# Optimization experiments

Hardware: AMD Instinct MI355X
Metric: run time of the kernel (lower is better)

Reference implementation:

```python
import jax, jax.numpy as jnp
import numpy as np

B, S, IN, H, OUT = 64, 512, 1024, 512, 512
EPS = 1e-5
ADAPTIVE_RATE = 0.01


def setup_inputs() -> dict:
    key = jax.random.key(0)
    ks = iter(jax.random.split(key, 64))

    def rn(shape, scale):
        return (jax.random.normal(next(ks), shape, jnp.float32) * scale)

    d = {}
    d["x"] = jax.random.normal(next(ks), (B, S, IN), jnp.float32)
    d["context"] = jax.random.normal(next(ks), (B, H), jnp.float32)
    d["state_importance"] = jnp.ones((1, H), jnp.float32)
    # embedding
    d["W_emb"], d["b_emb"] = rn((H, IN), 0.02), rn((H,), 0.01)
    # core layers: Linear + BatchNorm1d (gamma=1, beta=0 torch init)
    d["W0"], d["b0"] = rn((H, H), 0.03), rn((H,), 0.01)
    d["g0"], d["bt0"] = jnp.ones((H,), jnp.float32), jnp.zeros((H,), jnp.float32)
    d["W1"], d["b1"] = rn((H, H), 0.03), rn((H,), 0.01)
    d["g1"], d["bt1"] = jnp.ones((H,), jnp.float32), jnp.zeros((H,), jnp.float32)
    # two LSTMCells (hidden -> hidden), torch gate order i,f,g,o
    lstm_scale = 1.0 / np.sqrt(H)
    for l in range(2):
        d[f"Wih{l}"] = rn((4 * H, H), lstm_scale)
        d[f"Whh{l}"] = rn((4 * H, H), lstm_scale)
        d[f"bih{l}"] = rn((4 * H,), lstm_scale)
        d[f"bhh{l}"] = rn((4 * H,), lstm_scale)
    # compression gate: Linear(2H, H) + LayerNorm + Sigmoid
    d["Wc"], d["bc"] = rn((H, 2 * H), 0.02), rn((H,), 0.01)
    d["lnc_g"], d["lnc_b"] = jnp.ones((H,), jnp.float32), jnp.zeros((H,), jnp.float32)
    # importance generator: Linear, ReLU, Linear, LayerNorm, Sigmoid
    d["Wi1"], d["bi1"] = rn((H, H), 0.03), rn((H,), 0.01)
    d["Wi2"], d["bi2"] = rn((H, H), 0.03), rn((H,), 0.01)
    d["lni_g"], d["lni_b"] = jnp.ones((H,), jnp.float32), jnp.zeros((H,), jnp.float32)
    # final layer
    d["Wf"], d["bf"] = rn((OUT, H), 0.03), rn((OUT,), 0.01)
    return d


def _bn_channel_dim1(h, gamma, beta):
    # BatchNorm1d (training mode) on (B, S, H) with channel dim = dim 1 (S == num_features)
    m = h.mean(axis=(0, 2), keepdims=True)
    v = h.var(axis=(0, 2), keepdims=True)  # biased, like torch normalization
    return gamma[None, :, None] * (h - m) / jnp.sqrt(v + EPS) + beta[None, :, None]


def _ln(h, g, b):
    m = h.mean(-1, keepdims=True)
    v = h.var(-1, keepdims=True)
    return g * (h - m) / jnp.sqrt(v + EPS) + b


def _lstm_cell(xt, h, c, Wih, Whh, bih, bhh):
    z = xt @ Wih.T + bih + h @ Whh.T + bhh  # (B, 4H)
    i, f, g, o = jnp.split(z, 4, axis=-1)
    c = jax.nn.sigmoid(f) * c + jax.nn.sigmoid(i) * jnp.tanh(g)
    h = jax.nn.sigmoid(o) * jnp.tanh(c)
    return h, c


def reference(x, context, state_importance, W_emb, b_emb,
              W0, b0, g0, bt0, W1, b1, g1, bt1,
              Wih0, Whh0, bih0, bhh0, Wih1, Whh1, bih1, bhh1,
              Wc, bc, lnc_g, lnc_b, Wi1, bi1, Wi2, bi2, lni_g, lni_b,
              Wf, bf):
    h = x @ W_emb.T + b_emb  # (B, S, H)
    h = jax.nn.relu(_bn_channel_dim1(h @ W0.T + b0, g0, bt0))
    h = jax.nn.relu(_bn_channel_dim1(h @ W1.T + b1, g1, bt1))

    # stacked 2-layer LSTMCell over the sequence, keep only the final hidden
    zeros = jnp.zeros((B, H), h.dtype)

    def step(carry, xt):
        h0, c0, h1, c1 = carry
        h0, c0 = _lstm_cell(xt, h0, c0, Wih0, Whh0, bih0, bhh0)
        h1, c1 = _lstm_cell(h0, h1, c1, Wih1, Whh1, bih1, bhh1)
        return (h0, c0, h1, c1), None

    (h0, c0, h1, c1), _ = jax.lax.scan(step, (zeros, zeros, zeros, zeros),
                                       jnp.swapaxes(h, 0, 1))
    processed = h1  # (B, H)

    comp = jax.nn.sigmoid(_ln(jnp.concatenate([processed, context], axis=-1) @ Wc.T + bc,
                              lnc_g, lnc_b))
    compressed = processed * comp

    imp = jax.nn.sigmoid(_ln(jax.nn.relu(compressed @ Wi1.T + bi1) @ Wi2.T + bi2,
                             lni_g, lni_b))
    si_new = state_importance + ADAPTIVE_RATE * (
        jnp.abs(imp).mean(axis=0, keepdims=True) - state_importance)

    out = compressed @ Wf.T + bf
    return out, si_new
```

## Files before the change

### kernel.cpp

```cpp
#include <hip/hip_runtime.h>
#include <hip/hip_bf16.h>
#include <stdint.h>


typedef __attribute__((ext_vector_type(8))) short short8;
typedef __attribute__((ext_vector_type(4))) float floatx4;

__device__ inline float b2f(short u){
  union { float f; uint32_t i; } x; x.i = ((uint32_t)(uint16_t)u) << 16; return x.f;
}
__device__ inline short f2b(float f){
  union { float f; uint32_t i; } x; x.f = f;
  uint32_t r = (x.i + 0x7FFFu + ((x.i >> 16) & 1u)) >> 16;
  return (short)(uint16_t)r;
}
__device__ inline float sigm(float x){ return 1.0f / (1.0f + __expf(-x)); }

__device__ inline float blk_sum(float v, float* red){
  #pragma unroll
  for (int o = 32; o > 0; o >>= 1) v += __shfl_down(v, o, 64);
  int wv = threadIdx.x >> 6;
  __syncthreads();
  if ((threadIdx.x & 63) == 0) red[wv] = v;
  __syncthreads();
  return red[0] + red[1] + red[2] + red[3];
}

__device__ inline void stage16(const short* g, short* l){
  __builtin_amdgcn_global_load_lds(
      (const __attribute__((address_space(1))) void*)(uintptr_t)g,
      (__attribute__((address_space(3))) void*)(uintptr_t)l,
      16, 0, 0);
}


__global__ void set_flag(const unsigned* __restrict__ si_bits, unsigned* __restrict__ flag){
  if (threadIdx.x == 0 && blockIdx.x == 0)
    *flag = (si_bits[0] == 0x3F800000u) ? 1u : 0u;
}


__global__ __launch_bounds__(256) void convq(
    const unsigned* __restrict__ flag, int mode,
    const void* s0, long e0, short* d0, int n0,
    const void* s1, long e1, short* d1, int n1,
    const void* s2, long e2, short* d2, int n2,
    const void* s3, long e3, short* d3, int n3)
{
  const bool isf32 = (*flag != 0u);
  const int gid = blockIdx.x*256 + threadIdx.x;
  const int stride = gridDim.x*256;
  const void* ss[4] = {s0,s1,s2,s3};
  long ee[4]  = {e0,e1,e2,e3};
  short* dd[4] = {d0,d1,d2,d3};
  int nn[4]   = {n0,n1,n2,n3};
  for (int s = 0; s < 4; s++){
    if (!dd[s]) continue;
    if (mode == 1) {
      if (!isf32) continue;
      for (int i = gid; i < nn[s]; i += stride)
        dd[s][i] = ((const short*)ss[s])[ee[s] + i];
    } else if (isf32) {
      for (int i = gid; i < nn[s]; i += stride)
        dd[s][i] = f2b(((const float*)ss[s])[ee[s] + i]);
    } else {
      for (int i = gid; i < nn[s]; i += stride)
        dd[s][i] = ((const short*)ss[s])[ee[s] + i];
    }
  }
}


__global__ __launch_bounds__(256) void gemm_bt(
    const short* __restrict__ A, const short* __restrict__ A2, int splitRow,
    int lda, const short* __restrict__ W, const short* __restrict__ bias,
    short* __restrict__ C, int ldc, int row0, int K)
{
  __shared__ alignas(16) short As[128*32];
  __shared__ alignas(16) short Bs[128*32];
  const int tid  = threadIdx.x;
  const int lane = tid & 63;
  const int wave = tid >> 6;
  const int wm = wave >> 1, wn = wave & 1;
  const int bm = blockIdx.x, bn = blockIdx.y;
  const int R0 = row0 + bm*128;
  const short* Ab = (R0 < splitRow) ? A2 : A;

  floatx4 acc[4][4];
  #pragma unroll
  for (int i = 0; i < 4; i++)
    #pragma unroll
    for (int j = 0; j < 4; j++){ floatx4 z = {0.f,0.f,0.f,0.f}; acc[i][j] = z; }

  const short* Ag = Ab + (size_t)(R0 + (tid >> 2))*lda + (tid & 3)*8;
  const short* Wg = W  + (size_t)(bn*128 + (tid >> 2))*K + (tid & 3)*8;

  const int kk  = (lane >> 4) * 8;
  const int rA  = wm*64 + (lane & 15);
  const int rB  = wn*64 + (lane & 15);

  for (int k0 = 0; k0 < K; k0 += 32) {
    __syncthreads();
    stage16(Ag + k0,                  As + tid*8);
    stage16(Ag + k0 + (size_t)64*lda, As + 2048 + tid*8);
    stage16(Wg + k0,                  Bs + tid*8);
    stage16(Wg + k0 + (size_t)64*K,   Bs + 2048 + tid*8);
    __syncthreads();

    short8 af[4], bf[4];
    #pragma unroll
    for (int i = 0; i < 4; i++){
      af[i] = *(const short8*)&As[(rA + i*16)*32 + kk];
      bf[i] = *(const short8*)&Bs[(rB + i*16)*32 + kk];
    }
    #pragma unroll
    for (int i = 0; i < 4; i++)
      #pragma unroll
      for (int j = 0; j < 4; j++)
        acc[i][j] = __builtin_amdgcn_mfma_f32_16x16x32_bf16(af[i], bf[j], acc[i][j], 0, 0, 0);
  }

  const int crow0 = R0 + wm*64 + (lane >> 4)*4;
  const int ccol0 = bn*128 + wn*64;
  #pragma unroll
  for (int i = 0; i < 4; i++){
    #pragma unroll
    for (int j = 0; j < 4; j++){
      int col = ccol0 + j*16 + (lane & 15);
      float bv = b2f(bias[col]);
      #pragma unroll
      for (int r = 0; r < 4; r++){
        int row = crow0 + i*16 + r;
        C[(size_t)row*ldc + col] = f2b(acc[i][j][r] + bv);
      }
    }
  }
}


__global__ __launch_bounds__(256) void bn_relu(
    const short* __restrict__ X, const short* __restrict__ gamma,
    const short* __restrict__ beta, short* __restrict__ Y)
{
  const int s = blockIdx.x, tid = threadIdx.x;
  __shared__ float red[4];
  float s1 = 0.f, s2 = 0.f;
  for (int i = tid; i < 4096; i += 256){
    int b = i >> 6, c = i & 63;
    short8 v = *(const short8*)(X + ((size_t)(b*512 + s))*512 + c*8);
    #pragma unroll
    for (int u = 0; u < 8; u++){ float f = b2f(v[u]); s1 += f; s2 += f*f; }
  }
  s1 = blk_sum(s1, red);
  s2 = blk_sum(s2, red);
  float mean = s1 * (1.f/32768.f);
  float var  = fmaxf(s2 * (1.f/32768.f) - mean*mean, 0.f);
  float sc = b2f(gamma[s]) * rsqrtf(var + 1e-5f);
  float sh = b2f(beta[s]) - mean * sc;
  for (int i = tid; i < 4096; i += 256){
    int b = i >> 6, c = i & 63;
    size_t base = ((size_t)(b*512 + s))*512 + c*8;
    short8 v = *(const short8*)(X + base);
    short8 o;
    #pragma unroll
    for (int u = 0; u < 8; u++){
      float f = b2f(v[u]) * sc + sh;
      o[u] = f2b(fmaxf(f, 0.f));
    }
    *(short8*)(Y + base) = o;
  }
}


__global__ __launch_bounds__(256, 1) void lstm_persist(
    const short* __restrict__ Xseq,
    const short* __restrict__ Wih0, const short* __restrict__ Whh0,
    const short* __restrict__ bih0, const short* __restrict__ bhh0,
    const short* __restrict__ Wih1, const short* __restrict__ Whh1,
    const short* __restrict__ bih1, const short* __restrict__ bhh1,
    short* __restrict__ h0r,
    short* __restrict__ h1r,
    unsigned* __restrict__ slots)
{
  const int wg   = blockIdx.x;
  const int tid  = threadIdx.x;
  const int lane = tid & 63;
  const int wave = tid >> 6;
  const int l15  = lane & 15;
  const int quad = lane >> 4;
  const int kq   = quad * 8;

  __shared__ float zp[4*64*33];
  #define ZP(t,r,c) zp[((t)*64 + (r))*33 + (c)]

  const short* Wt = (wave==0) ? Wih0 : (wave==1) ? Whh0 : (wave==2) ? Wih1 : Whh1;
  short8 wreg[2][16];
  #pragma unroll
  for (int nt = 0; nt < 2; nt++){
    int g2 = nt*2 + (l15 >> 3);
    int ml = l15 & 7;
    const short* wrow = Wt + (size_t)(g2*512 + wg*8 + ml)*512 + kq;
    #pragma unroll
    for (int kk = 0; kk < 16; kk++)
      wreg[nt][kk] = *(const short8*)(wrow + kk*32);
  }

  const int bb  = tid >> 2;
  const int ml0 = (tid & 3) * 2;
  float bs0[4][2], bs1[4][2];
  #pragma unroll
  for (int g = 0; g < 4; g++)
    #pragma unroll
    for (int p = 0; p < 2; p++){
      int m = wg*8 + ml0 + p;
      bs0[g][p] = b2f(bih0[g*512+m]) + b2f(bhh0[g*512+m]);
      bs1[g][p] = b2f(bih1[g*512+m]) + b2f(bhh1[g*512+m]);
    }
  float c0[2] = {0.f, 0.f}, c1[2] = {0.f, 0.f};

  for (int it = 0; it <= 512; ++it){
    if (it > 0){
      if (wave == 0){
        for (;;){
          unsigned v = __hip_atomic_load(&slots[lane], __ATOMIC_RELAXED,
                                         __HIP_MEMORY_SCOPE_AGENT);
          if (__all((int)(v >= (unsigned)it))) break;
        }
      }
      __syncthreads();
      __builtin_amdgcn_fence(__ATOMIC_ACQUIRE, "agent");
    }

    floatx4 acc[4][2];
    #pragma unroll
    for (int mt = 0; mt < 4; mt++)
      #pragma unroll
      for (int nt = 0; nt < 2; nt++){ floatx4 z = {0.f,0.f,0.f,0.f}; acc[mt][nt] = z; }

    const bool act = (wave==0) ? (it < 512)
                   : (wave==1) ? (it >= 1 && it < 512)
                   : (wave==2) ? (it >= 1)
                   :             (it >= 2);
    if (act){
      const short* Ab;
      size_t rstride;
      if (wave == 0)      { Ab = Xseq + (size_t)it*512;               rstride = 262144; }
      else if (wave <= 2) { Ab = h0r + (size_t)((it-1)&1)*32768;      rstride = 512; }
      else                { Ab = h1r + (size_t)(it&1)*32768;          rstride = 512; }
      const short* ap[4];
      #pragma unroll
      for (int mt = 0; mt < 4; mt++)
        ap[mt] = Ab + (size_t)(mt*16 + l15)*rstride + kq;

      #pragma unroll
      for (int kk = 0; kk < 16; kk++){
        short8 af[4];
        #pragma unroll
        for (int mt = 0; mt < 4; mt++) af[mt] = *(const short8*)(ap[mt] + kk*32);
        #pragma unroll
        for (int mt = 0; mt < 4; mt++){
          acc[mt][0] = __builtin_amdgcn_mfma_f32_16x16x32_bf16(af[mt], wreg[0][kk], acc[mt][0], 0, 0, 0);
          acc[mt][1] = __builtin_amdgcn_mfma_f32_16x16x32_bf16(af[mt], wreg[1][kk], acc[mt][1], 0, 0, 0);
        }
      }
    }

    #pragma unroll
    for (int mt = 0; mt < 4; mt++)
      #pragma unroll
      for (int nt = 0; nt < 2; nt++)
        #pragma unroll
        for (int r = 0; r < 4; r++)
          ZP(wave, mt*16 + quad*4 + r, nt*16 + l15) = acc[mt][nt][r];
    __syncthreads();

    if (it < 512){
      float hv[2];
      #pragma unroll
      for (int p = 0; p < 2; p++){
        int ml = ml0 + p;
        float zi = ZP(0, bb,      ml) + ZP(1, bb,      ml) + bs0[0][p];
        float zf = ZP(0, bb,  8 + ml) + ZP(1, bb,  8 + ml) + bs0[1][p];
        float zg = ZP(0, bb, 16 + ml) + ZP(1, bb, 16 + ml) + bs0[2][p];
        float zo = ZP(0, bb, 24 + ml) + ZP(1, bb, 24 + ml) + bs0[3][p];
        c0[p] = sigm(zf)*c0[p] + sigm(zi)*tanhf(zg);
        hv[p] = sigm(zo)*tanhf(c0[p]);
      }
      unsigned pk = (unsigned)(uint16_t)f2b(hv[0]) | ((unsigned)(uint16_t)f2b(hv[1]) << 16);
      __hip_atomic_store((unsigned*)(h0r + (size_t)(it&1)*32768 + bb*512 + wg*8 + ml0),
                         pk, __ATOMIC_RELAXED, __HIP_MEMORY_SCOPE_AGENT);
    }
    if (it >= 1){
      float hv[2];
      #pragma unroll
      for (int p = 0; p < 2; p++){
        int ml = ml0 + p;
        float zi = ZP(2, bb,      ml) + ZP(3, bb,      ml) + bs1[0][p];
        float zf = ZP(2, bb,  8 + ml) + ZP(3, bb,  8 + ml) + bs1[1][p];
        float zg = ZP(2, bb, 16 + ml) + ZP(3, bb, 16 + ml) + bs1[2][p];
        float zo = ZP(2, bb, 24 + ml) + ZP(3, bb, 24 + ml) + bs1[3][p];
        c1[p] = sigm(zf)*c1[p] + sigm(zi)*tanhf(zg);
        hv[p] = sigm(zo)*tanhf(c1[p]);
      }
      unsigned pk = (unsigned)(uint16_t)f2b(hv[0]) | ((unsigned)(uint16_t)f2b(hv[1]) << 16);
      __hip_atomic_store((unsigned*)(h1r + (size_t)((it-1)&1)*32768 + bb*512 + wg*8 + ml0),
                         pk, __ATOMIC_RELAXED, __HIP_MEMORY_SCOPE_AGENT);
    }
    __syncthreads();
    if (tid == 0)
      __hip_atomic_store(&slots[wg], (unsigned)(it + 1),
                         __ATOMIC_RELAXED, __HIP_MEMORY_SCOPE_AGENT);
  }
  #undef ZP
}


__global__ __launch_bounds__(256) void head_gate_out(
    const short* __restrict__ h1, const short* __restrict__ ctx,
    const short* __restrict__ Wc, const short* __restrict__ bc,
    const short* __restrict__ lng, const short* __restrict__ lnb,
    const short* __restrict__ Wf, const short* __restrict__ bfb,
    short* __restrict__ compressed, void* __restrict__ outp,
    const unsigned* __restrict__ flag)
{
  const int b = blockIdx.x, tid = threadIdx.x;
  const bool isf32 = (*flag != 0u);
  __shared__ float xc[1024];
  __shared__ float cv[512];
  __shared__ float red[4];
  for (int i = tid; i < 512; i += 256) xc[i]       = b2f(h1 [b*512 + i]);
  for (int i = tid; i < 512; i += 256) xc[512 + i] = b2f(ctx[b*512 + i]);
  __syncthreads();
  float y[2];
  #pragma unroll
  for (int jj = 0; jj < 2; jj++){
    int j = tid + jj*256;
    const short* wr = Wc + (size_t)j*1024;
    float a = 0.f;
    for (int k = 0; k < 1024; k += 8){
      short8 wv = *(const short8*)(wr + k);
      #pragma unroll
      for (int u = 0; u < 8; u++) a += b2f(wv[u]) * xc[k + u];
    }
    y[jj] = a + b2f(bc[j]);
  }
  float s = blk_sum(y[0] + y[1], red);
  float mean = s * (1.f/512.f);
  float q = (y[0]-mean)*(y[0]-mean) + (y[1]-mean)*(y[1]-mean);
  q = blk_sum(q, red);
  float inv = rsqrtf(q * (1.f/512.f) + 1e-5f);
  #pragma unroll
  for (int jj = 0; jj < 2; jj++){
    int j = tid + jj*256;
    float v = (y[jj]-mean)*inv*b2f(lng[j]) + b2f(lnb[j]);
    float cm = xc[j] * sigm(v);
    cv[j] = cm;
    compressed[(size_t)b*512 + j] = f2b(cm);
  }
  __syncthreads();
  #pragma unroll
  for (int jj = 0; jj < 2; jj++){
    int j = tid + jj*256;
    const short* wr = Wf + (size_t)j*512;
    float a = 0.f;
    for (int k = 0; k < 512; k += 8){
      short8 wv = *(const short8*)(wr + k);
      #pragma unroll
      for (int u = 0; u < 8; u++) a += b2f(wv[u]) * cv[k + u];
    }
    float o = a + b2f(bfb[j]);
    if (isf32) ((float*)outp)[(size_t)b*512 + j] = o;
    else       ((short*)outp)[(size_t)b*512 + j] = f2b(o);
  }
}


__global__ __launch_bounds__(256) void head_imp(
    const short* __restrict__ compressed,
    const short* __restrict__ Wi1, const short* __restrict__ bi1,
    const short* __restrict__ Wi2, const short* __restrict__ bi2,
    const short* __restrict__ lng, const short* __restrict__ lnb,
    float* __restrict__ imp)
{
  const int b = blockIdx.x, tid = threadIdx.x;
  __shared__ float xr[512];
  __shared__ float t1[512];
  __shared__ float red[4];
  for (int i = tid; i < 512; i += 256) xr[i] = b2f(compressed[b*512 + i]);
  __syncthreads();
  #pragma unroll
  for (int jj = 0; jj < 2; jj++){
    int j = tid + jj*256;
    const short* wr = Wi1 + (size_t)j*512;
    float a = 0.f;
    for (int k = 0; k < 512; k += 8){
      short8 wv = *(const short8*)(wr + k);
      #pragma unroll
      for (int u = 0; u < 8; u++) a += b2f(wv[u]) * xr[k + u];
    }
    t1[j] = fmaxf(a + b2f(bi1[j]), 0.f);
  }
  __syncthreads();
  float y[2];
  #pragma unroll
  for (int jj = 0; jj < 2; jj++){
    int j = tid + jj*256;
    const short* wr = Wi2 + (size_t)j*512;
    float a = 0.f;
    for (int k = 0; k < 512; k += 8){
      short8 wv = *(const short8*)(wr + k);
      #pragma unroll
      for (int u = 0; u < 8; u++) a += b2f(wv[u]) * t1[k + u];
    }
    y[jj] = a + b2f(bi2[j]);
  }
  float s = blk_sum(y[0] + y[1], red);
  float mean = s * (1.f/512.f);
  float q = (y[0]-mean)*(y[0]-mean) + (y[1]-mean)*(y[1]-mean);
  q = blk_sum(q, red);
  float inv = rsqrtf(q * (1.f/512.f) + 1e-5f);
  #pragma unroll
  for (int jj = 0; jj < 2; jj++){
    int j = tid + jj*256;
    imp[(size_t)b*512 + j] = sigm((y[jj]-mean)*inv*b2f(lng[j]) + b2f(lnb[j]));
  }
}


__global__ __launch_bounds__(256) void head_si(
    const float* __restrict__ imp, const short* __restrict__ si,
    void* __restrict__ outp, const unsigned* __restrict__ flag)
{
  int tid = threadIdx.x;
  const bool isf32 = (*flag != 0u);
  #pragma unroll
  for (int mm = 0; mm < 2; mm++){
    int m = tid + mm*256;
    float s = 0.f;
    for (int b = 0; b < 64; b++) s += fabsf(imp[(size_t)b*512 + m]);
    float mean = s * (1.f/64.f);
    float sv = b2f(si[m]);
    float o = sv + 0.01f*(mean - sv);
    if (isf32) ((float*)outp)[32768 + m] = o;
    else       ((short*)outp)[32768 + m] = f2b(o);
  }
}


extern "C" void kernel_launch(void* const* d_in, const int* in_sizes, int n_in,
                              void* d_out, int out_size, void* d_ws, size_t ws_size,
                              hipStream_t stream)
{
  (void)in_sizes; (void)n_in; (void)out_size; (void)ws_size;
  char* ws = (char*)d_ws;
  unsigned* slots  = (unsigned*)(ws);
  unsigned* flag   = (unsigned*)(ws + 4096);
  short*    xStage = (short*)(ws + 8192);
  short*    ring   = (short*)(ws + 270336);
  short*    comp   = (short*)(ws + 925696);
  float*    impb   = (float*)(ws + 991232);
  short*    SA     = (short*)(ws + 1122304);

  short* h0r = ring;
  short* h1r = ring + 65536;

  short* aWemb = SA + 0;
  short* aW0   = SA + 524288;
  short* aW1   = SA + 786432;
  short* aWih0 = SA + 1048576;
  short* aWhh0 = SA + 2097152;
  short* aWih1 = SA + 3145728;
  short* aWhh1 = SA + 4194304;
  short* aWc   = SA + 5242880;
  short* aWi1  = SA + 5767168;
  short* aWi2  = SA + 6029312;
  short* aWf   = SA + 6291456;
  short* V     = SA + 6553600;
  short* abemb = V + 0;     short* ab0  = V + 512;   short* ag0  = V + 1024;
  short* abt0  = V + 1536;  short* ab1  = V + 2048;  short* ag1  = V + 2560;
  short* abt1  = V + 3072;  short* abih0= V + 3584;  short* abhh0= V + 5632;
  short* abih1 = V + 7680;  short* abhh1= V + 9728;  short* abc  = V + 11776;
  short* alncg = V + 12288; short* alncb= V + 12800; short* abi1 = V + 13312;
  short* abi2  = V + 13824; short* alnig= V + 14336; short* alnib= V + 14848;
  short* abfb  = V + 15360; short* actx = V + 15872; short* asi  = V + 48640;

  short* xb  = (short*)d_in[0];
  short* hL0 = xb + 16777216;

  hipMemsetAsync(slots, 0, 4096, stream);
  set_flag<<<1, 64, 0, stream>>>((const unsigned*)d_in[2], flag);

  dim3 blk(256);
  convq<<<256, blk, 0, stream>>>(flag, 0,
      d_in[0], 0, xStage, 65536, nullptr,0,nullptr,0, nullptr,0,nullptr,0, nullptr,0,nullptr,0);
  for (long n0 = 65536; n0 < 33554432; n0 <<= 1) {
    int blocks = (int)((n0 + 1023) / 1024); if (blocks > 4096) blocks = 4096;
    convq<<<blocks, blk, 0, stream>>>(flag, 0,
        d_in[0], n0, xb + n0, (int)n0, nullptr,0,nullptr,0, nullptr,0,nullptr,0, nullptr,0,nullptr,0);
  }
  convq<<<64, blk, 0, stream>>>(flag, 1,
      xStage, 0, xb, 65536, nullptr,0,nullptr,0, nullptr,0,nullptr,0, nullptr,0,nullptr,0);

  convq<<<1024, blk, 0, stream>>>(flag, 0,
      d_in[3], 0, aWemb, 524288,  d_in[5], 0, aW0, 262144,
      d_in[9], 0, aW1,   262144,  d_in[21],0, aWc, 524288);
  convq<<<2048, blk, 0, stream>>>(flag, 0,
      d_in[13],0, aWih0, 1048576, d_in[14],0, aWhh0, 1048576,
      d_in[17],0, aWih1, 1048576, d_in[18],0, aWhh1, 1048576);
  convq<<<1024, blk, 0, stream>>>(flag, 0,
      d_in[25],0, aWi1, 262144,   d_in[27],0, aWi2, 262144,
      d_in[31],0, aWf,  262144,   d_in[1], 0, actx, 32768);
  convq<<<8, blk, 0, stream>>>(flag, 0,
      d_in[4], 0, abemb, 512,  d_in[6], 0, ab0, 512,
      d_in[7], 0, ag0,   512,  d_in[8], 0, abt0, 512);
  convq<<<8, blk, 0, stream>>>(flag, 0,
      d_in[10],0, ab1, 512,  d_in[11],0, ag1, 512,
      d_in[12],0, abt1,512,  d_in[22],0, abc, 512);
  convq<<<8, blk, 0, stream>>>(flag, 0,
      d_in[15],0, abih0, 2048,  d_in[16],0, abhh0, 2048,
      d_in[19],0, abih1, 2048,  d_in[20],0, abhh1, 2048);
  convq<<<8, blk, 0, stream>>>(flag, 0,
      d_in[23],0, alncg, 512,  d_in[24],0, alncb, 512,
      d_in[26],0, abi1,  512,  d_in[28],0, abi2,  512);
  convq<<<8, blk, 0, stream>>>(flag, 0,
      d_in[29],0, alnig, 512,  d_in[30],0, alnib, 512,
      d_in[32],0, abfb,  512,  d_in[2], 0, asi,   512);

  gemm_bt<<<dim3(1, 4), blk, 0, stream>>>(xb, xb, 0, 1024, aWemb, abemb,
                                          xStage, 512, 0, 1024);
  for (int r0 = 128; r0 < 32768; r0 <<= 1) {
    gemm_bt<<<dim3(r0/128, 4), blk, 0, stream>>>(xb, xb, 0, 1024, aWemb, abemb,
                                                 xb, 512, r0, 1024);
  }
  gemm_bt<<<dim3(256, 4), blk, 0, stream>>>(xb, xStage, 128, 512, aW0, ab0,
                                            hL0, 512, 0, 512);
  bn_relu<<<512, blk, 0, stream>>>(hL0, ag0, abt0, hL0);
  gemm_bt<<<dim3(256, 4), blk, 0, stream>>>(hL0, hL0, 0, 512, aW1, ab1,
                                            xb, 512, 0, 512);
  bn_relu<<<512, blk, 0, stream>>>(xb, ag1, abt1, xb);

  lstm_persist<<<64, blk, 0, stream>>>(xb, aWih0, aWhh0, abih0, abhh0,
                                       aWih1, aWhh1, abih1, abhh1,
                                       h0r, h1r, slots);

  head_gate_out<<<64, blk, 0, stream>>>(h1r + 32768, actx, aWc, abc, alncg, alncb,
                                        aWf, abfb, comp, d_out, flag);
  head_imp<<<64, blk, 0, stream>>>(comp, aWi1, abi1, aWi2, abi2, alnig, alnib, impb);
  head_si<<<1, blk, 0, stream>>>(impb, asi, d_out, flag);
}
```

Baseline: 8.416 ms.

## Use system-scope coherent loads for the LSTM ring and pad the sync slots

```diff
diff --git a/kernel.cpp b/kernel.cpp
--- a/kernel.cpp
+++ b/kernel.cpp
@@ -31,6 +31,14 @@
       (const __attribute__((address_space(1))) void*)(uintptr_t)g,
       (__attribute__((address_space(3))) void*)(uintptr_t)l,
       16, 0, 0);
+}
+
+__device__ inline short8 ld_coh8(const short* p){
+  const unsigned long long* q = (const unsigned long long*)p;
+  union { unsigned long long u[2]; short8 v; } c;
+  c.u[0] = __hip_atomic_load(q,     __ATOMIC_RELAXED, __HIP_MEMORY_SCOPE_SYSTEM);
+  c.u[1] = __hip_atomic_load(q + 1, __ATOMIC_RELAXED, __HIP_MEMORY_SCOPE_SYSTEM);
+  return c.v;
 }
 
 
@@ -222,13 +230,12 @@
     if (it > 0){
       if (wave == 0){
         for (;;){
-          unsigned v = __hip_atomic_load(&slots[lane], __ATOMIC_RELAXED,
-                                         __HIP_MEMORY_SCOPE_AGENT);
+          unsigned v = __hip_atomic_load(&slots[lane*32], __ATOMIC_RELAXED,
+                                         __HIP_MEMORY_SCOPE_SYSTEM);
           if (__all((int)(v >= (unsigned)it))) break;
         }
       }
       __syncthreads();
-      __builtin_amdgcn_fence(__ATOMIC_ACQUIRE, "agent");
     }
 
     floatx4 acc[4][2];
@@ -242,25 +249,40 @@
                    : (wave==2) ? (it >= 1)
                    :             (it >= 2);
     if (act){
-      const short* Ab;
-      size_t rstride;
-      if (wave == 0)      { Ab = Xseq + (size_t)it*512;               rstride = 262144; }
-      else if (wave <= 2) { Ab = h0r + (size_t)((it-1)&1)*32768;      rstride = 512; }
-      else                { Ab = h1r + (size_t)(it&1)*32768;          rstride = 512; }
-      const short* ap[4];
-      #pragma unroll
-      for (int mt = 0; mt < 4; mt++)
-        ap[mt] = Ab + (size_t)(mt*16 + l15)*rstride + kq;
-
-      #pragma unroll
-      for (int kk = 0; kk < 16; kk++){
-        short8 af[4];
+      if (wave == 0){
+        const short* Ab = Xseq + (size_t)it*512;
+        const short* ap[4];
         #pragma unroll
-        for (int mt = 0; mt < 4; mt++) af[mt] = *(const short8*)(ap[mt] + kk*32);
+        for (int mt = 0; mt < 4; mt++)
+          ap[mt] = Ab + (size_t)(mt*16 + l15)*262144 + kq;
         #pragma unroll
-        for (int mt = 0; mt < 4; mt++){
-          acc[mt][0] = __builtin_amdgcn_mfma_f32_16x16x32_bf16(af[mt], wreg[0][kk], acc[mt][0], 0, 0, 0);
-          acc[mt][1] = __builtin_amdgcn_mfma_f32_16x16x32_bf16(af[mt], wreg[1][kk], acc[mt][1], 0, 0, 0);
+        for (int kk = 0; kk < 16; kk++){
+          short8 af[4];
+          #pragma unroll
+          for (int mt = 0; mt < 4; mt++) af[mt] = *(const short8*)(ap[mt] + kk*32);
+          #pragma unroll
+          for (int mt = 0; mt < 4; mt++){
+            acc[mt][0] = __builtin_amdgcn_mfma_f32_16x16x32_bf16(af[mt], wreg[0][kk], acc[mt][0], 0, 0, 0);
+            acc[mt][1] = __builtin_amdgcn_mfma_f32_16x16x32_bf16(af[mt], wreg[1][kk], acc[mt][1], 0, 0, 0);
+          }
+        }
+      } else {
+        const short* Ab = (wave <= 2) ? h0r + (size_t)((it-1)&1)*32768
+                                      : h1r + (size_t)(it&1)*32768;
+        const short* ap[4];
+        #pragma unroll
+        for (int mt = 0; mt < 4; mt++)
+          ap[mt] = Ab + (size_t)(mt*16 + l15)*512 + kq;
+        #pragma unroll
+        for (int kk = 0; kk < 16; kk++){
+          short8 af[4];
+          #pragma unroll
+          for (int mt = 0; mt < 4; mt++) af[mt] = ld_coh8(ap[mt] + kk*32);
+          #pragma unroll
+          for (int mt = 0; mt < 4; mt++){
+            acc[mt][0] = __builtin_amdgcn_mfma_f32_16x16x32_bf16(af[mt], wreg[0][kk], acc[mt][0], 0, 0, 0);
+            acc[mt][1] = __builtin_amdgcn_mfma_f32_16x16x32_bf16(af[mt], wreg[1][kk], acc[mt][1], 0, 0, 0);
+          }
         }
       }
     }
@@ -288,7 +310,7 @@
       }
       unsigned pk = (unsigned)(uint16_t)f2b(hv[0]) | ((unsigned)(uint16_t)f2b(hv[1]) << 16);
       __hip_atomic_store((unsigned*)(h0r + (size_t)(it&1)*32768 + bb*512 + wg*8 + ml0),
-                         pk, __ATOMIC_RELAXED, __HIP_MEMORY_SCOPE_AGENT);
+                         pk, __ATOMIC_RELAXED, __HIP_MEMORY_SCOPE_SYSTEM);
     }
     if (it >= 1){
       float hv[2];
@@ -304,12 +326,12 @@
       }
       unsigned pk = (unsigned)(uint16_t)f2b(hv[0]) | ((unsigned)(uint16_t)f2b(hv[1]) << 16);
       __hip_atomic_store((unsigned*)(h1r + (size_t)((it-1)&1)*32768 + bb*512 + wg*8 + ml0),
-                         pk, __ATOMIC_RELAXED, __HIP_MEMORY_SCOPE_AGENT);
+                         pk, __ATOMIC_RELAXED, __HIP_MEMORY_SCOPE_SYSTEM);
     }
     __syncthreads();
     if (tid == 0)
-      __hip_atomic_store(&slots[wg], (unsigned)(it + 1),
-                         __ATOMIC_RELAXED, __HIP_MEMORY_SCOPE_AGENT);
+      __hip_atomic_store(&slots[wg*32], (unsigned)(it + 1),
+                         __ATOMIC_RELAXED, __HIP_MEMORY_SCOPE_SYSTEM);
   }
   #undef ZP
 }
@@ -454,12 +476,12 @@
   (void)in_sizes; (void)n_in; (void)out_size; (void)ws_size;
   char* ws = (char*)d_ws;
   unsigned* slots  = (unsigned*)(ws);
-  unsigned* flag   = (unsigned*)(ws + 4096);
-  short*    xStage = (short*)(ws + 8192);
-  short*    ring   = (short*)(ws + 270336);
-  short*    comp   = (short*)(ws + 925696);
-  float*    impb   = (float*)(ws + 991232);
-  short*    SA     = (short*)(ws + 1122304);
+  unsigned* flag   = (unsigned*)(ws + 8192);
+  short*    xStage = (short*)(ws + 12288);
+  short*    ring   = (short*)(ws + 274432);
+  short*    comp   = (short*)(ws + 536576);
+  float*    impb   = (float*)(ws + 602112);
+  short*    SA     = (short*)(ws + 733184);
 
   short* h0r = ring;
   short* h1r = ring + 65536;
@@ -487,7 +509,7 @@
   short* xb  = (short*)d_in[0];
   short* hL0 = xb + 16777216;
 
-  hipMemsetAsync(slots, 0, 4096, stream);
+  hipMemsetAsync(slots, 0, 8192, stream);
   set_flag<<<1, 64, 0, stream>>>((const unsigned*)d_in[2], flag);
 
   dim3 blk(256);
```

Result: slower. 10.96 ms (+30.2%).
